# Optimization experiments

Hardware: AMD Instinct MI355X
Metric: run time of the kernel (lower is better)

## Reference

```python
import jax, jax.numpy as jnp
import numpy as np

D = 512  # token_dim == hidden_dim
K = 65536  # number of trajectory tokens


def safe_normalize(v, eps=1e-6):
    n = jnp.linalg.norm(v, axis=-1, keepdims=True)
    ok = n > eps
    e1 = jnp.zeros_like(v).at[..., 0].set(1.0)
    return jnp.where(ok, v / jnp.maximum(n, eps), e1)


def rot6d_to_matrix(x, eps=1e-6):
    # x: (K, 6) -> R: (K, 3, 3), rows (a1, b2, a3)
    a1 = safe_normalize(x[..., 0:3], eps)
    a2 = x[..., 3:6]
    proj = jnp.sum(a1 * a2, axis=-1, keepdims=True) * a1
    b2 = safe_normalize(a2 - proj, eps)
    a3 = safe_normalize(jnp.cross(a1, b2), eps)
    b2 = safe_normalize(jnp.cross(a3, a1), eps)
    return jnp.stack((a1, b2, a3), axis=-2)


def geodesic_angle(R_pred, R_gt, eps=1e-8):
    # RtR = R_gt^T @ R_pred, per-element (K,3,3)
    RtR = jnp.einsum('kji,kjl->kil', R_gt, R_pred)
    trace = RtR[..., 0, 0] + RtR[..., 1, 1] + RtR[..., 2, 2]
    c = jnp.clip((trace - 1.0) * 0.5, -1.0 + 1e-6, 1.0 - 1e-6)
    skew = RtR - jnp.swapaxes(RtR, -1, -2)
    v = jnp.stack([skew[..., 2, 1], skew[..., 0, 2], skew[..., 1, 0]], axis=-1)
    s = 0.5 * jnp.linalg.norm(v, axis=-1) + eps
    return jnp.arctan2(s, c)


def huber(pred, target, beta, mask):
    # smooth-L1 with beta, masked mean (denominator = clamped mask sum)
    d = jnp.abs(pred - target)
    l = jnp.where(d < beta, 0.5 * d * d / beta, d - 0.5 * beta) * mask
    return l.sum() / jnp.maximum(mask.sum(), 1.0)


def rot_loss_fn(pred, gt):
    # pred, gt: (K, 12) = [L rot6d(6), R rot6d(6)]
    Lp, Rp = pred[:, :6], pred[:, 6:]
    Lt, Rt = gt[:, :6], gt[:, 6:]
    Lvalid = jnp.all(Lt != -1000.0, axis=-1)
    Rvalid = jnp.all(Rt != -1000.0, axis=-1)
    safe6 = jnp.array([1.0, 0.0, 0.0, 0.0, 1.0, 0.0], pred.dtype)
    Lt = jnp.where(Lvalid[:, None], Lt, safe6)
    Rt = jnp.where(Rvalid[:, None], Rt, safe6)
    ang_L = geodesic_angle(rot6d_to_matrix(Lp), rot6d_to_matrix(Lt))
    ang_R = geodesic_angle(rot6d_to_matrix(Rp), rot6d_to_matrix(Rt))
    wL = Lvalid.astype(pred.dtype)
    wR = Rvalid.astype(pred.dtype)
    denom = jnp.maximum(wL.sum() + wR.sum(), 1e-8)
    num = jnp.sum(wL * jnp.where(Lvalid, ang_L, 0.0)) + jnp.sum(wR * jnp.where(Rvalid, ang_R, 0.0))
    return num / denom


def _heads(hidden_states, w1, b1, w2, b2, w3, b3):
    # 4 stacked MLPs (m = time, coord, coord2d, quat), torch Linear layout (out, in)
    h1 = jax.nn.relu(jnp.einsum('kc,mhc->mkh', hidden_states, w1) + b1[:, None, :])
    h2 = jax.nn.relu(jnp.einsum('mkh,mgh->mkg', h1, w2) + b2[:, None, :])
    pred_time = h2[0] @ w3[0:1].T + b3[0:1]      # (K, 1)
    pred_coords = h2[1] @ w3[1:7].T + b3[1:7]    # (K, 6)
    pred_2d = h2[2] @ w3[7:11].T + b3[7:11]      # (K, 4)
    pred_quat = h2[3] @ w3[11:23].T + b3[11:23]  # (K, 12)
    return pred_time, pred_coords, pred_2d, pred_quat


def _loss(pred_time, pred_coords, pred_2d, pred_quat, gt,
          beta_3d=0.07, beta_2d=0.02, beta_time=3.0, sigma_time=3.0):
    time_gt = gt[:, 0:1]
    time_valid = (time_gt != -1000.0).astype(jnp.float32)
    xyz_gt = gt[:, 1:7]
    xyz_valid = (xyz_gt != -1000.0).astype(jnp.float32)
    uv_gt = gt[:, 7:11]
    uv_valid = (uv_gt != -1000.0).astype(jnp.float32)
    quat_gt = gt[:, 11:23]
    quat_valid = (quat_gt != -1000.0).astype(jnp.float32)

    time_loss = huber(pred_time, time_gt, beta_time, time_valid)

    dt = jnp.abs(pred_time - time_gt)
    w_t = jnp.where(time_valid.sum() > 0,
                    jnp.exp(-0.5 * (dt / sigma_time) ** 2) * time_valid,
                    jnp.ones_like(pred_time))  # (K, 1), broadcasts over feature dims

    loss_3d = huber(pred_coords, xyz_gt, beta_3d, xyz_valid * w_t)
    loss_2d = huber(pred_2d / 1408.0, uv_gt / 1408.0, beta_2d, uv_valid * w_t)
    quat_huber = huber(pred_quat, quat_gt, 0.2, quat_valid * w_t)
    rot_l = 0.15 * rot_loss_fn(pred_quat, quat_gt)

    return 1.0 * time_loss + 2.0 * loss_3d + 0.5 * loss_2d + 0.5 * quat_huber + rot_l


def setup_inputs() -> dict:
    key = jax.random.key(0)
    ks = jax.random.split(key, 6)
    s = 1.0 / np.sqrt(D)
    return {
        'hidden_states': jax.random.normal(ks[0], (K, D), jnp.float32),
        'gt_traj': jax.random.uniform(ks[1], (K, 23), jnp.float32),
        'w1': jax.random.normal(ks[2], (4, D, D), jnp.float32) * s,
        'b1': jnp.zeros((4, D), jnp.float32),
        'w2': jax.random.normal(ks[3], (4, D, D), jnp.float32) * s,
        'b2': jnp.zeros((4, D), jnp.float32),
        'w3': jax.random.normal(ks[4], (23, D), jnp.float32) * s,
        'b3': jnp.zeros((23,), jnp.float32),
    }


def reference(hidden_states, gt_traj, w1, b1, w2, b2, w3, b3):
    pred_time, pred_coords, pred_2d, pred_quat = _heads(hidden_states, w1, b1, w2, b2, w3, b3)
    total_loss = _loss(pred_time, pred_coords, pred_2d, pred_quat, gt_traj)
    packed = jnp.concatenate(
        [pred_coords.reshape(-1, 2, 3), pred_quat.reshape(-1, 2, 6)], axis=-1
    ).reshape(-1, 18)
    return pred_time, packed, total_loss
```

## Files before the change

### kernel.cpp

```cpp
#include <hip/hip_runtime.h>
#include <math.h>


#define KROWS 65536
#define DH 512

typedef _Float16 f16;
typedef _Float16 half8 __attribute__((ext_vector_type(8)));
typedef float floatx4 __attribute__((ext_vector_type(4)));

#define WS_WF16   0
#define WS_W3F16  4194304
#define WS_PRED2D 4227072
#define WS_PART   5275648

__global__ __launch_bounds__(256) void convert_weights(
    const float* __restrict__ w1, const float* __restrict__ w2,
    const float* __restrict__ w3, f16* __restrict__ wf16, f16* __restrict__ w3f16)
{
  int t = blockIdx.x * 256 + threadIdx.x;
  if (t < 262144) {
    int ml = t >> 15;
    int mm = ml >> 1, l = ml & 1;
    int r = t & 32767;
    int fb = r >> 6;
    int lane = r & 63;
    int nt = fb >> 4, kq = fb & 15;
    int n = nt * 16 + (lane & 15);
    int k = kq * 32 + (lane >> 4) * 8;
    const float* src = (l ? w2 : w1) + (size_t)mm * 262144 + n * 512 + k;
    floatx4 u0 = *(const floatx4*)(src);
    floatx4 u1 = *(const floatx4*)(src + 4);
    half8 h;
    h[0] = (f16)u0[0]; h[1] = (f16)u0[1]; h[2] = (f16)u0[2]; h[3] = (f16)u0[3];
    h[4] = (f16)u1[0]; h[5] = (f16)u1[1]; h[6] = (f16)u1[2]; h[7] = (f16)u1[3];
    *(half8*)(wf16 + (size_t)ml * 262144 + fb * 512 + lane * 8) = h;
  } else {
    int j = t - 262144;
    if (j < 23 * DH) w3f16[j] = (f16)w3[j];
  }
}

extern __shared__ unsigned char smem[];

__global__ __launch_bounds__(512, 4) void fused_kernel(
    const float* __restrict__ hidden,
    const f16* __restrict__ wf16,
    const f16* __restrict__ w3f16,
    const float* __restrict__ b1g,
    const float* __restrict__ b2g,
    const float* __restrict__ b3g,
    float* __restrict__ dout,
    float* __restrict__ pred2d)
{
  const int bid = blockIdx.x;
  const int rr  = bid & 7;
  const int m   = rr >> 1;
  const int row_tile = ((bid >> 3) << 1) | (rr & 1);
  const int r0  = row_tile * 64;
  const int tid = threadIdx.x;
  const int w   = __builtin_amdgcn_readfirstlane(tid >> 6);
  const int lane = tid & 63;
  const int l15 = lane & 15;
  const int lg  = lane >> 4;

  unsigned char* h1b = smem;
  unsigned char* stg = smem + 65536;

  const int arow = l15 * 128;
  const int ao   = (lg * 16) ^ ((l15 & 7) << 4);
  const f16* bptr = wf16 + (size_t)(m * 2) * 262144 + lane * 8;
  const int srow = tid >> 3;
  const int swaddr = srow * 128 + (((tid & 7) * 16) ^ ((srow & 7) << 4));
  const float* hrow = hidden + (size_t)(r0 + srow) * DH + (tid & 7) * 8;

  floatx4 s0, s1;
  auto sload = [&](int kc) {
    const float* p = hrow + kc * 64;
    s0 = *(const floatx4*)(p);
    s1 = *(const floatx4*)(p + 4);
  };
  auto swrite = [&](int buf) {
    half8 p0;
    p0[0] = (f16)s0[0]; p0[1] = (f16)s0[1]; p0[2] = (f16)s0[2]; p0[3] = (f16)s0[3];
    p0[4] = (f16)s1[0]; p0[5] = (f16)s1[1]; p0[6] = (f16)s1[2]; p0[7] = (f16)s1[3];
    *(half8*)(stg + buf * 8192 + swaddr) = p0;
  };
  auto aread = [&](const unsigned char* chunk, int mt, int kq) -> half8 {
    return *(const half8*)(chunk + mt * 2048 + arow + (ao ^ (kq << 6)));
  };
  auto bload = [&](int l, int g, int nt) -> half8 {
    return *(const half8*)(bptr + l * 262144 + ((w * 4 + nt) * 16 + g) * 512);
  };

  floatx4 acc[4][4];
  const floatx4 zf = {0.f, 0.f, 0.f, 0.f};

  sload(0); swrite(0);
#pragma unroll
  for (int mt = 0; mt < 4; ++mt)
#pragma unroll
    for (int nt = 0; nt < 4; ++nt) acc[mt][nt] = zf;
  __syncthreads();

#pragma unroll
  for (int g = 0; g < 16; ++g) {
    const int kc = g >> 1;
    if ((g & 1) == 0 && kc < 7) sload(kc + 1);
    half8 b0 = bload(0, g, 0), b1 = bload(0, g, 1),
          b2 = bload(0, g, 2), b3 = bload(0, g, 3);
    const unsigned char* chunk = stg + (kc & 1) * 8192;
#pragma unroll
    for (int mt = 0; mt < 4; ++mt) {
      half8 a = aread(chunk, mt, g & 1);
      acc[mt][0] = __builtin_amdgcn_mfma_f32_16x16x32_f16(a, b0, acc[mt][0], 0, 0, 0);
      acc[mt][1] = __builtin_amdgcn_mfma_f32_16x16x32_f16(a, b1, acc[mt][1], 0, 0, 0);
      acc[mt][2] = __builtin_amdgcn_mfma_f32_16x16x32_f16(a, b2, acc[mt][2], 0, 0, 0);
      acc[mt][3] = __builtin_amdgcn_mfma_f32_16x16x32_f16(a, b3, acc[mt][3], 0, 0, 0);
    }
    if ((g & 1) == 1 && kc < 7) {
      swrite((kc + 1) & 1);
      __syncthreads();
    }
  }

  {
    unsigned char* myc = h1b + w * 8192;
#pragma unroll
    for (int nt = 0; nt < 4; ++nt) {
      const float bv = b1g[m * DH + w * 64 + nt * 16 + l15];
      const int cb = 2 * (nt * 16 + l15);
#pragma unroll
      for (int mt = 0; mt < 4; ++mt)
#pragma unroll
        for (int j = 0; j < 4; ++j) {
          float v = fmaxf(acc[mt][nt][j] + bv, 0.f);
          int row = mt * 16 + 4 * lg + j;
          *(f16*)(myc + row * 128 + (cb ^ ((row & 7) << 4))) = (f16)v;
        }
    }
  }
  __syncthreads();

#pragma unroll
  for (int mt = 0; mt < 4; ++mt)
#pragma unroll
    for (int nt = 0; nt < 4; ++nt) acc[mt][nt] = zf;

#pragma unroll
  for (int g = 0; g < 16; ++g) {
    half8 b0 = bload(1, g, 0), b1 = bload(1, g, 1),
          b2 = bload(1, g, 2), b3 = bload(1, g, 3);
    const unsigned char* chunk = h1b + (g >> 1) * 8192;
#pragma unroll
    for (int mt = 0; mt < 4; ++mt) {
      half8 a = aread(chunk, mt, g & 1);
      acc[mt][0] = __builtin_amdgcn_mfma_f32_16x16x32_f16(a, b0, acc[mt][0], 0, 0, 0);
      acc[mt][1] = __builtin_amdgcn_mfma_f32_16x16x32_f16(a, b1, acc[mt][1], 0, 0, 0);
      acc[mt][2] = __builtin_amdgcn_mfma_f32_16x16x32_f16(a, b2, acc[mt][2], 0, 0, 0);
      acc[mt][3] = __builtin_amdgcn_mfma_f32_16x16x32_f16(a, b3, acc[mt][3], 0, 0, 0);
    }
  }
  __syncthreads();

  {
    unsigned char* myc = h1b + w * 8192;
#pragma unroll
    for (int nt = 0; nt < 4; ++nt) {
      const float bv = b2g[m * DH + w * 64 + nt * 16 + l15];
      const int cb = 2 * (nt * 16 + l15);
#pragma unroll
      for (int mt = 0; mt < 4; ++mt)
#pragma unroll
        for (int j = 0; j < 4; ++j) {
          float v = fmaxf(acc[mt][nt][j] + bv, 0.f);
          int row = mt * 16 + 4 * lg + j;
          *(f16*)(myc + row * 128 + (cb ^ ((row & 7) << 4))) = (f16)v;
        }
    }
  }
  __syncthreads();

  if (w < 4) {
    const int base_m = (m == 0) ? 0 : (m == 1) ? 1 : (m == 2) ? 7 : 11;
    const int cnt_m  = (m == 0) ? 1 : (m == 1) ? 6 : (m == 2) ? 4 : 12;
    const bool ovalid = l15 < cnt_m;
    const f16* w3row = w3f16 + (size_t)(base_m + (ovalid ? l15 : 0)) * DH;
    const half8 hz = {(f16)0, (f16)0, (f16)0, (f16)0, (f16)0, (f16)0, (f16)0, (f16)0};
    floatx4 acc3 = zf;
#pragma unroll
    for (int q = 0; q < 16; ++q) {
      half8 ah = aread(h1b + (q >> 1) * 8192, w, q & 1);
      half8 wv = ovalid ? *(const half8*)(w3row + q * 32 + lg * 8) : hz;
      acc3 = __builtin_amdgcn_mfma_f32_16x16x32_f16(ah, wv, acc3, 0, 0, 0);
    }
    if (ovalid) {
      const float bo = b3g[base_m + l15];
#pragma unroll
      for (int j = 0; j < 4; ++j) {
        const int row = r0 + w * 16 + 4 * lg + j;
        const float v = acc3[j] + bo;
        if (m == 0)      { if (l15 == 0) dout[row] = v; }
        else if (m == 1) { dout[KROWS + row * 18 + (l15 < 3 ? l15 : l15 + 6)] = v; }
        else if (m == 2) { pred2d[row * 4 + l15] = v; }
        else             { dout[KROWS + row * 18 + (l15 < 6 ? l15 + 3 : l15 + 6)] = v; }
      }
    }
  }
}

__device__ __forceinline__ void safe_norm3(float x, float y, float z, float* o) {
  float n = sqrtf(x * x + y * y + z * z);
  if (n > 1e-6f) { o[0] = x / n; o[1] = y / n; o[2] = z / n; }
  else           { o[0] = 1.f;   o[1] = 0.f;   o[2] = 0.f; }
}

__device__ __forceinline__ void rot6d(const float* x, float* R) {
  float a1[3]; safe_norm3(x[0], x[1], x[2], a1);
  float d = a1[0] * x[3] + a1[1] * x[4] + a1[2] * x[5];
  float b2[3]; safe_norm3(x[3] - d * a1[0], x[4] - d * a1[1], x[5] - d * a1[2], b2);
  float a3[3];
  safe_norm3(a1[1] * b2[2] - a1[2] * b2[1],
             a1[2] * b2[0] - a1[0] * b2[2],
             a1[0] * b2[1] - a1[1] * b2[0], a3);
  float bb[3];
  safe_norm3(a3[1] * a1[2] - a3[2] * a1[1],
             a3[2] * a1[0] - a3[0] * a1[2],
             a3[0] * a1[1] - a3[1] * a1[0], bb);
  R[0] = a1[0]; R[1] = a1[1]; R[2] = a1[2];
  R[3] = bb[0]; R[4] = bb[1]; R[5] = bb[2];
  R[6] = a3[0]; R[7] = a3[1]; R[8] = a3[2];
}

__device__ __forceinline__ float geo_angle(const float* P, const float* G) {
  float M[9];
#pragma unroll
  for (int i = 0; i < 3; ++i)
#pragma unroll
    for (int l = 0; l < 3; ++l)
      M[i * 3 + l] = G[0 + i] * P[0 + l] + G[3 + i] * P[3 + l] + G[6 + i] * P[6 + l];
  float tr = M[0] + M[4] + M[8];
  float c = fminf(fmaxf((tr - 1.f) * 0.5f, -1.f + 1e-6f), 1.f - 1e-6f);
  float v0 = M[7] - M[5], v1 = M[2] - M[6], v2 = M[3] - M[1];
  float s = 0.5f * sqrtf(v0 * v0 + v1 * v1 + v2 * v2) + 1e-8f;
  return atan2f(s, c);
}

__global__ __launch_bounds__(256) void loss_partial(
    const float* __restrict__ gt, const float* __restrict__ dout,
    const float* __restrict__ pred2d, float* __restrict__ partials)
{
  const int r = blockIdx.x * 256 + threadIdx.x;
  const float* g  = gt + (size_t)r * 23;
  const float* pk = dout + KROWS + (size_t)r * 18;
  float a[17];

  const float pt = dout[r];
  const float tg = g[0];
  const float tv = (tg != -1000.f) ? 1.f : 0.f;
  const float dt = fabsf(pt - tg);
  a[0] = ((dt < 3.f) ? (0.5f * dt * dt / 3.f) : (dt - 1.5f)) * tv;
  a[1] = tv;
  a[2] = tv;
  const float wt = expf(-0.5f * (dt / 3.f) * (dt / 3.f)) * tv;

  float n3T = 0.f, d3T = 0.f, n3F = 0.f, d3F = 0.f;
#pragma unroll
  for (int j = 0; j < 6; ++j) {
    const float p = pk[j < 3 ? j : j + 6];
    const float q = g[1 + j];
    const float val = (q != -1000.f) ? 1.f : 0.f;
    const float d = fabsf(p - q);
    const float l = (d < 0.07f) ? (0.5f * d * d / 0.07f) : (d - 0.035f);
    n3T += l * val * wt; d3T += val * wt; n3F += l * val; d3F += val;
  }
  a[3] = n3T; a[4] = d3T; a[5] = n3F; a[6] = d3F;

  float n2T = 0.f, d2T = 0.f, n2F = 0.f, d2F = 0.f;
#pragma unroll
  for (int j = 0; j < 4; ++j) {
    const float p = pred2d[(size_t)r * 4 + j];
    const float q = g[7 + j];
    const float val = (q != -1000.f) ? 1.f : 0.f;
    const float d = fabsf(p / 1408.f - q / 1408.f);
    const float l = (d < 0.02f) ? (0.5f * d * d / 0.02f) : (d - 0.01f);
    n2T += l * val * wt; d2T += val * wt; n2F += l * val; d2F += val;
  }
  a[7] = n2T; a[8] = d2T; a[9] = n2F; a[10] = d2F;

  float qp[12];
#pragma unroll
  for (int j = 0; j < 12; ++j) qp[j] = pk[j < 6 ? j + 3 : j + 6];
  float nqT = 0.f, dqT = 0.f, nqF = 0.f, dqF = 0.f;
#pragma unroll
  for (int j = 0; j < 12; ++j) {
    const float q = g[11 + j];
    const float val = (q != -1000.f) ? 1.f : 0.f;
    const float d = fabsf(qp[j] - q);
    const float l = (d < 0.2f) ? (0.5f * d * d / 0.2f) : (d - 0.1f);
    nqT += l * val * wt; dqT += val * wt; nqF += l * val; dqF += val;
  }
  a[11] = nqT; a[12] = dqT; a[13] = nqF; a[14] = dqF;

  bool Lv = true, Rv = true;
#pragma unroll
  for (int j = 0; j < 6; ++j) {
    if (g[11 + j] == -1000.f) Lv = false;
    if (g[17 + j] == -1000.f) Rv = false;
  }
  const float safe6[6] = {1.f, 0.f, 0.f, 0.f, 1.f, 0.f};
  float Lt[6], Rt[6];
#pragma unroll
  for (int j = 0; j < 6; ++j) {
    Lt[j] = Lv ? g[11 + j] : safe6[j];
    Rt[j] = Rv ? g[17 + j] : safe6[j];
  }
  float Rp[9], Rg[9];
  rot6d(qp, Rp);     rot6d(Lt, Rg);
  const float angL = geo_angle(Rp, Rg);
  rot6d(qp + 6, Rp); rot6d(Rt, Rg);
  const float angR = geo_angle(Rp, Rg);
  a[15] = (Lv ? angL : 0.f) + (Rv ? angR : 0.f);
  a[16] = (Lv ? 1.f : 0.f) + (Rv ? 1.f : 0.f);

#pragma unroll
  for (int i = 0; i < 17; ++i) {
    float v = a[i];
#pragma unroll
    for (int off = 32; off > 0; off >>= 1) v += __shfl_down(v, off, 64);
    a[i] = v;
  }
  __shared__ float red[4][17];
  if ((threadIdx.x & 63) == 0) {
    const int wv = threadIdx.x >> 6;
#pragma unroll
    for (int i = 0; i < 17; ++i) red[wv][i] = a[i];
  }
  __syncthreads();
  if (threadIdx.x < 17)
    partials[blockIdx.x * 20 + threadIdx.x] =
        red[0][threadIdx.x] + red[1][threadIdx.x] + red[2][threadIdx.x] + red[3][threadIdx.x];
}

__global__ void loss_final(const float* __restrict__ partials, float* __restrict__ dout)
{
  __shared__ float s[17];
  const int i = threadIdx.x;
  if (i < 17) {
    float v = 0.f;
    for (int b = 0; b < 256; ++b) v += partials[b * 20 + i];
    s[i] = v;
  }
  __syncthreads();
  if (i == 0) {
    const bool flag = s[2] > 0.f;
    const float time_loss = s[0] / fmaxf(s[1], 1.f);
    const float l3 = flag ? s[3] / fmaxf(s[4], 1.f) : s[5] / fmaxf(s[6], 1.f);
    const float l2 = flag ? s[7] / fmaxf(s[8], 1.f) : s[9] / fmaxf(s[10], 1.f);
    const float lq = flag ? s[11] / fmaxf(s[12], 1.f) : s[13] / fmaxf(s[14], 1.f);
    const float rot = 0.15f * (s[15] / fmaxf(s[16], 1e-8f));
    dout[19 * KROWS] = time_loss + 2.f * l3 + 0.5f * l2 + 0.5f * lq + rot;
  }
}

extern "C" void kernel_launch(void* const* d_in, const int* in_sizes, int n_in,
                              void* d_out, int out_size, void* d_ws, size_t ws_size,
                              hipStream_t stream) {
  (void)in_sizes; (void)n_in; (void)out_size; (void)ws_size;
  const float* hidden = (const float*)d_in[0];
  const float* gt     = (const float*)d_in[1];
  const float* w1     = (const float*)d_in[2];
  const float* b1     = (const float*)d_in[3];
  const float* w2     = (const float*)d_in[4];
  const float* b2     = (const float*)d_in[5];
  const float* w3     = (const float*)d_in[6];
  const float* b3     = (const float*)d_in[7];
  float* dout = (float*)d_out;

  unsigned char* ws = (unsigned char*)d_ws;
  f16*   wf16     = (f16*)(ws + WS_WF16);
  f16*   w3f16    = (f16*)(ws + WS_W3F16);
  float* pred2d   = (float*)(ws + WS_PRED2D);
  float* partials = (float*)(ws + WS_PART);

  static bool attr_done = false;
  if (!attr_done) {
    hipFuncSetAttribute(reinterpret_cast<const void*>(fused_kernel),
                        hipFuncAttributeMaxDynamicSharedMemorySize, 81920);
    attr_done = true;
  }

  convert_weights<<<1070, 256, 0, stream>>>(w1, w2, w3, wf16, w3f16);
  fused_kernel<<<4096, 512, 81920, stream>>>(hidden, wf16, w3f16, b1, b2, b3, dout, pred2d);
  loss_partial<<<256, 256, 0, stream>>>(gt, dout, pred2d, partials);
  loss_final<<<1, 64, 0, stream>>>(partials, dout);
}
```

Baseline: 361.3 us.

## Process all four heads per block, loading hidden tile once into LDS

```diff
diff --git a/kernel.cpp b/kernel.cpp
--- a/kernel.cpp
+++ b/kernel.cpp
@@ -43,7 +43,7 @@
 
 extern __shared__ unsigned char smem[];
 
-__global__ __launch_bounds__(512, 4) void fused_kernel(
+__global__ __launch_bounds__(512, 2) void fused_kernel(
     const float* __restrict__ hidden,
     const f16* __restrict__ wf16,
     const f16* __restrict__ w3f16,
@@ -53,159 +53,167 @@
     float* __restrict__ dout,
     float* __restrict__ pred2d)
 {
-  const int bid = blockIdx.x;
-  const int rr  = bid & 7;
-  const int m   = rr >> 1;
-  const int row_tile = ((bid >> 3) << 1) | (rr & 1);
-  const int r0  = row_tile * 64;
+  const int r0  = blockIdx.x * 64;
   const int tid = threadIdx.x;
   const int w   = __builtin_amdgcn_readfirstlane(tid >> 6);
   const int lane = tid & 63;
   const int l15 = lane & 15;
   const int lg  = lane >> 4;
 
-  unsigned char* h1b = smem;
-  unsigned char* stg = smem + 65536;
+  unsigned char* Ab = smem;
+  unsigned char* hb = smem + 65536;
 
   const int arow = l15 * 128;
   const int ao   = (lg * 16) ^ ((l15 & 7) << 4);
-  const f16* bptr = wf16 + (size_t)(m * 2) * 262144 + lane * 8;
-  const int srow = tid >> 3;
-  const int swaddr = srow * 128 + (((tid & 7) * 16) ^ ((srow & 7) << 4));
-  const float* hrow = hidden + (size_t)(r0 + srow) * DH + (tid & 7) * 8;
-
-  floatx4 s0, s1;
-  auto sload = [&](int kc) {
-    const float* p = hrow + kc * 64;
-    s0 = *(const floatx4*)(p);
-    s1 = *(const floatx4*)(p + 4);
-  };
-  auto swrite = [&](int buf) {
-    half8 p0;
-    p0[0] = (f16)s0[0]; p0[1] = (f16)s0[1]; p0[2] = (f16)s0[2]; p0[3] = (f16)s0[3];
-    p0[4] = (f16)s1[0]; p0[5] = (f16)s1[1]; p0[6] = (f16)s1[2]; p0[7] = (f16)s1[3];
-    *(half8*)(stg + buf * 8192 + swaddr) = p0;
-  };
   auto aread = [&](const unsigned char* chunk, int mt, int kq) -> half8 {
     return *(const half8*)(chunk + mt * 2048 + arow + (ao ^ (kq << 6)));
   };
-  auto bload = [&](int l, int g, int nt) -> half8 {
-    return *(const half8*)(bptr + l * 262144 + ((w * 4 + nt) * 16 + g) * 512);
+  const f16* bptr = wf16 + lane * 8;
+  auto bload = [&](int mm, int l, int g, int nt) -> half8 {
+    return *(const half8*)(bptr + ((mm * 2 + l)) * 262144
+                           + ((w * 4 + nt) * 16 + g) * 512);
   };
+
+  {
+    const int row = tid >> 3;
+    const int cg  = tid & 7;
+    const int sw  = ((cg * 16) ^ ((row & 7) << 4));
+    const float* hr = hidden + (size_t)(r0 + row) * DH + cg * 8;
+    unsigned char* dst = Ab + row * 128 + sw;
+#pragma unroll
+    for (int kc = 0; kc < 8; ++kc) {
+      floatx4 u0 = *(const floatx4*)(hr + kc * 64);
+      floatx4 u1 = *(const floatx4*)(hr + kc * 64 + 4);
+      half8 p;
+      p[0] = (f16)u0[0]; p[1] = (f16)u0[1]; p[2] = (f16)u0[2]; p[3] = (f16)u0[3];
+      p[4] = (f16)u1[0]; p[5] = (f16)u1[1]; p[6] = (f16)u1[2]; p[7] = (f16)u1[3];
+      *(half8*)(dst + kc * 8192) = p;
+    }
+  }
 
   floatx4 acc[4][4];
   const floatx4 zf = {0.f, 0.f, 0.f, 0.f};
-
-  sload(0); swrite(0);
-#pragma unroll
-  for (int mt = 0; mt < 4; ++mt)
-#pragma unroll
-    for (int nt = 0; nt < 4; ++nt) acc[mt][nt] = zf;
+  const half8 hz = {(f16)0, (f16)0, (f16)0, (f16)0, (f16)0, (f16)0, (f16)0, (f16)0};
+
   __syncthreads();
 
-#pragma unroll
-  for (int g = 0; g < 16; ++g) {
-    const int kc = g >> 1;
-    if ((g & 1) == 0 && kc < 7) sload(kc + 1);
-    half8 b0 = bload(0, g, 0), b1 = bload(0, g, 1),
-          b2 = bload(0, g, 2), b3 = bload(0, g, 3);
-    const unsigned char* chunk = stg + (kc & 1) * 8192;
-#pragma unroll
-    for (int mt = 0; mt < 4; ++mt) {
-      half8 a = aread(chunk, mt, g & 1);
-      acc[mt][0] = __builtin_amdgcn_mfma_f32_16x16x32_f16(a, b0, acc[mt][0], 0, 0, 0);
-      acc[mt][1] = __builtin_amdgcn_mfma_f32_16x16x32_f16(a, b1, acc[mt][1], 0, 0, 0);
-      acc[mt][2] = __builtin_amdgcn_mfma_f32_16x16x32_f16(a, b2, acc[mt][2], 0, 0, 0);
-      acc[mt][3] = __builtin_amdgcn_mfma_f32_16x16x32_f16(a, b3, acc[mt][3], 0, 0, 0);
-    }
-    if ((g & 1) == 1 && kc < 7) {
-      swrite((kc + 1) & 1);
-      __syncthreads();
-    }
-  }
-
-  {
-    unsigned char* myc = h1b + w * 8192;
-#pragma unroll
-    for (int nt = 0; nt < 4; ++nt) {
-      const float bv = b1g[m * DH + w * 64 + nt * 16 + l15];
-      const int cb = 2 * (nt * 16 + l15);
-#pragma unroll
-      for (int mt = 0; mt < 4; ++mt)
+#pragma unroll 1
+  for (int m = 0; m < 4; ++m) {
+#pragma unroll
+    for (int mt = 0; mt < 4; ++mt)
+#pragma unroll
+      for (int nt = 0; nt < 4; ++nt) acc[mt][nt] = zf;
+
+    half8 c0 = bload(m, 0, 0, 0), c1 = bload(m, 0, 0, 1),
+          c2 = bload(m, 0, 0, 2), c3 = bload(m, 0, 0, 3);
+#pragma unroll 1
+    for (int g = 0; g < 16; ++g) {
+      half8 n0, n1, n2, n3;
+      if (g < 15) {
+        n0 = bload(m, 0, g + 1, 0); n1 = bload(m, 0, g + 1, 1);
+        n2 = bload(m, 0, g + 1, 2); n3 = bload(m, 0, g + 1, 3);
+      }
+      const unsigned char* chunk = Ab + (g >> 1) * 8192;
+#pragma unroll
+      for (int mt = 0; mt < 4; ++mt) {
+        half8 a = aread(chunk, mt, g & 1);
+        acc[mt][0] = __builtin_amdgcn_mfma_f32_16x16x32_f16(a, c0, acc[mt][0], 0, 0, 0);
+        acc[mt][1] = __builtin_amdgcn_mfma_f32_16x16x32_f16(a, c1, acc[mt][1], 0, 0, 0);
+        acc[mt][2] = __builtin_amdgcn_mfma_f32_16x16x32_f16(a, c2, acc[mt][2], 0, 0, 0);
+        acc[mt][3] = __builtin_amdgcn_mfma_f32_16x16x32_f16(a, c3, acc[mt][3], 0, 0, 0);
+      }
+      c0 = n0; c1 = n1; c2 = n2; c3 = n3;
+    }
+
+    {
+      unsigned char* myc = hb + w * 8192;
+#pragma unroll
+      for (int nt = 0; nt < 4; ++nt) {
+        const float bv = b1g[m * DH + w * 64 + nt * 16 + l15];
+        const int cb = 2 * (nt * 16 + l15);
+#pragma unroll
+        for (int mt = 0; mt < 4; ++mt)
+#pragma unroll
+          for (int j = 0; j < 4; ++j) {
+            float v = fmaxf(acc[mt][nt][j] + bv, 0.f);
+            int row = mt * 16 + 4 * lg + j;
+            *(f16*)(myc + row * 128 + (cb ^ ((row & 7) << 4))) = (f16)v;
+          }
+      }
+    }
+    __syncthreads();
+
+#pragma unroll
+    for (int mt = 0; mt < 4; ++mt)
+#pragma unroll
+      for (int nt = 0; nt < 4; ++nt) acc[mt][nt] = zf;
+
+    c0 = bload(m, 1, 0, 0); c1 = bload(m, 1, 0, 1);
+    c2 = bload(m, 1, 0, 2); c3 = bload(m, 1, 0, 3);
+#pragma unroll 1
+    for (int g = 0; g < 16; ++g) {
+      half8 n0, n1, n2, n3;
+      if (g < 15) {
+        n0 = bload(m, 1, g + 1, 0); n1 = bload(m, 1, g + 1, 1);
+        n2 = bload(m, 1, g + 1, 2); n3 = bload(m, 1, g + 1, 3);
+      }
+      const unsigned char* chunk = hb + (g >> 1) * 8192;
+#pragma unroll
+      for (int mt = 0; mt < 4; ++mt) {
+        half8 a = aread(chunk, mt, g & 1);
+        acc[mt][0] = __builtin_amdgcn_mfma_f32_16x16x32_f16(a, c0, acc[mt][0], 0, 0, 0);
+        acc[mt][1] = __builtin_amdgcn_mfma_f32_16x16x32_f16(a, c1, acc[mt][1], 0, 0, 0);
+        acc[mt][2] = __builtin_amdgcn_mfma_f32_16x16x32_f16(a, c2, acc[mt][2], 0, 0, 0);
+        acc[mt][3] = __builtin_amdgcn_mfma_f32_16x16x32_f16(a, c3, acc[mt][3], 0, 0, 0);
+      }
+      c0 = n0; c1 = n1; c2 = n2; c3 = n3;
+    }
+    __syncthreads();
+
+    {
+      unsigned char* myc = hb + w * 8192;
+#pragma unroll
+      for (int nt = 0; nt < 4; ++nt) {
+        const float bv = b2g[m * DH + w * 64 + nt * 16 + l15];
+        const int cb = 2 * (nt * 16 + l15);
+#pragma unroll
+        for (int mt = 0; mt < 4; ++mt)
+#pragma unroll
+          for (int j = 0; j < 4; ++j) {
+            float v = fmaxf(acc[mt][nt][j] + bv, 0.f);
+            int row = mt * 16 + 4 * lg + j;
+            *(f16*)(myc + row * 128 + (cb ^ ((row & 7) << 4))) = (f16)v;
+          }
+      }
+    }
+    __syncthreads();
+
+    if (w < 4) {
+      const int base_m = (m == 0) ? 0 : (m == 1) ? 1 : (m == 2) ? 7 : 11;
+      const int cnt_m  = (m == 0) ? 1 : (m == 1) ? 6 : (m == 2) ? 4 : 12;
+      const bool ovalid = l15 < cnt_m;
+      const f16* w3row = w3f16 + (size_t)(base_m + (ovalid ? l15 : 0)) * DH;
+      floatx4 acc3 = zf;
+#pragma unroll
+      for (int q = 0; q < 16; ++q) {
+        half8 ah = aread(hb + (q >> 1) * 8192, w, q & 1);
+        half8 wv = ovalid ? *(const half8*)(w3row + q * 32 + lg * 8) : hz;
+        acc3 = __builtin_amdgcn_mfma_f32_16x16x32_f16(ah, wv, acc3, 0, 0, 0);
+      }
+      if (ovalid) {
+        const float bo = b3g[base_m + l15];
 #pragma unroll
         for (int j = 0; j < 4; ++j) {
-          float v = fmaxf(acc[mt][nt][j] + bv, 0.f);
-          int row = mt * 16 + 4 * lg + j;
-          *(f16*)(myc + row * 128 + (cb ^ ((row & 7) << 4))) = (f16)v;
+          const int row = r0 + w * 16 + 4 * lg + j;
+          const float v = acc3[j] + bo;
+          if (m == 0)      { if (l15 == 0) dout[row] = v; }
+          else if (m == 1) { dout[KROWS + row * 18 + (l15 < 3 ? l15 : l15 + 6)] = v; }
+          else if (m == 2) { pred2d[row * 4 + l15] = v; }
+          else             { dout[KROWS + row * 18 + (l15 < 6 ? l15 + 3 : l15 + 6)] = v; }
         }
-    }
-  }
-  __syncthreads();
-
-#pragma unroll
-  for (int mt = 0; mt < 4; ++mt)
-#pragma unroll
-    for (int nt = 0; nt < 4; ++nt) acc[mt][nt] = zf;
-
-#pragma unroll
-  for (int g = 0; g < 16; ++g) {
-    half8 b0 = bload(1, g, 0), b1 = bload(1, g, 1),
-          b2 = bload(1, g, 2), b3 = bload(1, g, 3);
-    const unsigned char* chunk = h1b + (g >> 1) * 8192;
-#pragma unroll
-    for (int mt = 0; mt < 4; ++mt) {
-      half8 a = aread(chunk, mt, g & 1);
-      acc[mt][0] = __builtin_amdgcn_mfma_f32_16x16x32_f16(a, b0, acc[mt][0], 0, 0, 0);
-      acc[mt][1] = __builtin_amdgcn_mfma_f32_16x16x32_f16(a, b1, acc[mt][1], 0, 0, 0);
-      acc[mt][2] = __builtin_amdgcn_mfma_f32_16x16x32_f16(a, b2, acc[mt][2], 0, 0, 0);
-      acc[mt][3] = __builtin_amdgcn_mfma_f32_16x16x32_f16(a, b3, acc[mt][3], 0, 0, 0);
-    }
-  }
-  __syncthreads();
-
-  {
-    unsigned char* myc = h1b + w * 8192;
-#pragma unroll
-    for (int nt = 0; nt < 4; ++nt) {
-      const float bv = b2g[m * DH + w * 64 + nt * 16 + l15];
-      const int cb = 2 * (nt * 16 + l15);
-#pragma unroll
-      for (int mt = 0; mt < 4; ++mt)
-#pragma unroll
-        for (int j = 0; j < 4; ++j) {
-          float v = fmaxf(acc[mt][nt][j] + bv, 0.f);
-          int row = mt * 16 + 4 * lg + j;
-          *(f16*)(myc + row * 128 + (cb ^ ((row & 7) << 4))) = (f16)v;
-        }
-    }
-  }
-  __syncthreads();
-
-  if (w < 4) {
-    const int base_m = (m == 0) ? 0 : (m == 1) ? 1 : (m == 2) ? 7 : 11;
-    const int cnt_m  = (m == 0) ? 1 : (m == 1) ? 6 : (m == 2) ? 4 : 12;
-    const bool ovalid = l15 < cnt_m;
-    const f16* w3row = w3f16 + (size_t)(base_m + (ovalid ? l15 : 0)) * DH;
-    const half8 hz = {(f16)0, (f16)0, (f16)0, (f16)0, (f16)0, (f16)0, (f16)0, (f16)0};
-    floatx4 acc3 = zf;
-#pragma unroll
-    for (int q = 0; q < 16; ++q) {
-      half8 ah = aread(h1b + (q >> 1) * 8192, w, q & 1);
-      half8 wv = ovalid ? *(const half8*)(w3row + q * 32 + lg * 8) : hz;
-      acc3 = __builtin_amdgcn_mfma_f32_16x16x32_f16(ah, wv, acc3, 0, 0, 0);
-    }
-    if (ovalid) {
-      const float bo = b3g[base_m + l15];
-#pragma unroll
-      for (int j = 0; j < 4; ++j) {
-        const int row = r0 + w * 16 + 4 * lg + j;
-        const float v = acc3[j] + bo;
-        if (m == 0)      { if (l15 == 0) dout[row] = v; }
-        else if (m == 1) { dout[KROWS + row * 18 + (l15 < 3 ? l15 : l15 + 6)] = v; }
-        else if (m == 2) { pred2d[row * 4 + l15] = v; }
-        else             { dout[KROWS + row * 18 + (l15 < 6 ? l15 + 3 : l15 + 6)] = v; }
-      }
-    }
+      }
+    }
+    __syncthreads();
   }
 }
 
@@ -386,12 +394,12 @@
   static bool attr_done = false;
   if (!attr_done) {
     hipFuncSetAttribute(reinterpret_cast<const void*>(fused_kernel),
-                        hipFuncAttributeMaxDynamicSharedMemorySize, 81920);
+                        hipFuncAttributeMaxDynamicSharedMemorySize, 131072);
     attr_done = true;
   }
 
   convert_weights<<<1070, 256, 0, stream>>>(w1, w2, w3, wf16, w3f16);
-  fused_kernel<<<4096, 512, 81920, stream>>>(hidden, wf16, w3f16, b1, b2, b3, dout, pred2d);
+  fused_kernel<<<1024, 512, 131072, stream>>>(hidden, wf16, w3f16, b1, b2, b3, dout, pred2d);
   loss_partial<<<256, 256, 0, stream>>>(gt, dout, pred2d, partials);
   loss_final<<<1, 64, 0, stream>>>(partials, dout);
 }
```

After: 370.6 us. 1.03x slower.
